# Performance work log

Hardware: AMD Instinct MI355X
Metric: run time of the kernel (lower is better)

The kernel has to match this reference:

```python
import jax, jax.numpy as jnp
import numpy as np

N = 100000   # nodes
E = 1600000  # edges
F = 256      # feature_dim
H = 64       # hidden_dim == out_channels
HEADS = 1


def setup_inputs() -> dict:
    key = jax.random.key(0)
    ks = jax.random.split(key, 12)
    x = jax.random.normal(ks[0], (N, F), dtype=jnp.float32)
    edge_index = jax.random.randint(ks[1], (2, E), 0, N, dtype=jnp.int32)
    s = 0.05
    params = {
        'W_proj': jax.random.normal(ks[2], (F, H), dtype=jnp.float32) * s,
        'b_proj': jnp.zeros((H,), dtype=jnp.float32),
        'Wq1': jax.random.normal(ks[3], (H, HEADS * H), dtype=jnp.float32) * s,
        'Wk1': jax.random.normal(ks[4], (H, HEADS * H), dtype=jnp.float32) * s,
        'Wv1': jax.random.normal(ks[5], (H, HEADS * H), dtype=jnp.float32) * s,
        'Wq2': jax.random.normal(ks[6], (H, HEADS * H), dtype=jnp.float32) * s,
        'Wk2': jax.random.normal(ks[7], (H, HEADS * H), dtype=jnp.float32) * s,
        'Wv2': jax.random.normal(ks[8], (H, HEADS * H), dtype=jnp.float32) * s,
        'W_sig': jax.random.normal(ks[9], (H, 1), dtype=jnp.float32) * s,
        'b_sig': jnp.zeros((1,), dtype=jnp.float32),
    }
    return {'x': x, 'edge_index': edge_index, **params}


def _gat_layer(x, src, dst, Wq, Wk, Wv):
    # x: [N, H]; src/dst: [E] (edge_index[0]=source j, edge_index[1]=dest i)
    n = x.shape[0]
    q = (x @ Wq).reshape(n, HEADS, H)
    k = (x @ Wk).reshape(n, HEADS, H)
    v = (x @ Wv).reshape(n, HEADS, H)
    # edge-wise scores: (q_i * k_j).sum(-1) / sqrt(out_channels)
    scores = jnp.einsum('ehc,ehc->eh', q[dst], k[src]) / np.float32(np.sqrt(H))
    alpha = jax.nn.relu(scores)                                  # [E, HEADS]
    # segment softmax over destination neighborhoods (numerically stable)
    m = jax.ops.segment_max(alpha, dst, num_segments=n)          # [N, HEADS]
    m = jnp.where(jnp.isfinite(m), m, jnp.float32(0.0))
    e = jnp.exp(alpha - m[dst])
    denom = jax.ops.segment_sum(e, dst, num_segments=n)
    a = e / (denom[dst] + jnp.float32(1e-16))                    # [E, HEADS]
    # scatter-weighted sum of values to destinations
    out = jax.ops.segment_sum(v[src] * a[:, :, None], dst, num_segments=n)
    return out.mean(axis=1), a                                   # [N, H], [E, HEADS]


def reference(x, edge_index, W_proj, b_proj, Wq1, Wk1, Wv1, Wq2, Wk2, Wv2, W_sig, b_sig):
    src, dst = edge_index[0], edge_index[1]
    h = jax.nn.gelu(x @ W_proj + b_proj, approximate=False)
    h, attn1 = _gat_layer(h, src, dst, Wq1, Wk1, Wv1)
    h = jax.nn.gelu(h, approximate=False)
    h, attn2 = _gat_layer(h, src, dst, Wq2, Wk2, Wv2)
    signals = h @ W_sig + b_sig                                  # [N, 1]
    return signals, attn1, attn2
```

## Files before the change

### kernel.cpp

```cpp
#include <hip/hip_runtime.h>
#include <hip/hip_fp16.h>
#include <math.h>

#define FF 256
#define HH 64

typedef __attribute__((ext_vector_type(8))) short short8;
typedef __attribute__((ext_vector_type(4))) float f32x4;

__device__ __forceinline__ float gelu_f(float x) {
    float ax = fabsf(x) * 0.70710678118654752f;
    float t = __builtin_amdgcn_rcpf(fmaf(0.3275911f, ax, 1.0f));
    float poly = t * fmaf(t, fmaf(t, fmaf(t, fmaf(t, 1.061405429f, -1.453152027f),
                  1.421413741f), -0.284496736f), 0.254829592f);
    float er = 1.0f - poly * __expf(-ax * ax);
    er = (x < 0.f) ? -er : er;
    return 0.5f * x * (1.0f + er);
}

__device__ __forceinline__ unsigned short bf16rne(float f) {
    unsigned u = __float_as_uint(f);
    unsigned r = u + 0x7FFFu + ((u >> 16) & 1u);
    return (unsigned short)(r >> 16);
}

__device__ __forceinline__ void bf16split(float f, short& hi, short& lo) {
    unsigned u = __float_as_uint(f);
    unsigned r = u + 0x7FFFu + ((u >> 16) & 1u);
    hi = (short)(r >> 16);
    float fh = __uint_as_float(r & 0xFFFF0000u);
    float fl = f - fh;
    unsigned u2 = __float_as_uint(fl);
    unsigned r2 = u2 + 0x7FFFu + ((u2 >> 16) & 1u);
    lo = (short)(r2 >> 16);
}

__device__ __forceinline__ __half2 shfl_xor_h2(__half2 v, int off) {
    union { __half2 h; int i; } u;
    u.h = v;
    u.i = __shfl_xor(u.i, off, 64);
    return u.h;
}

__global__ __launch_bounds__(256) void k_wprep(
        const float* __restrict__ Wp,
        const float* __restrict__ Wq1, const float* __restrict__ Wk1, const float* __restrict__ Wv1,
        const float* __restrict__ Wq2, const float* __restrict__ Wk2, const float* __restrict__ Wv2,
        short* __restrict__ wf) {
    int total = 16384 + 6 * 4096;
    for (int gid = blockIdx.x * 256 + threadIdx.x; gid < total; gid += gridDim.x * 256) {
        const float* W;
        int fid, hibase, lobase;
        if (gid < 16384) {
            W = Wp; fid = gid; hibase = 0; lobase = 16384;
        } else {
            int t = gid - 16384;
            int m = t >> 12;
            fid = t & 4095;
            switch (m) {
                case 0: W = Wq1; break;
                case 1: W = Wk1; break;
                case 2: W = Wv1; break;
                case 3: W = Wq2; break;
                case 4: W = Wk2; break;
                default: W = Wv2; break;
            }
            hibase = 32768 + m * 8192;
            lobase = hibase + 4096;
        }
        int j    = fid & 7;
        int lane = (fid >> 3) & 63;
        int ct   = (fid >> 9) & 3;
        int s    = fid >> 11;
        int k    = s * 32 + (lane >> 4) * 8 + j;
        int col  = ct * 16 + (lane & 15);
        short hi, lo;
        bf16split(W[k * HH + col], hi, lo);
        wf[hibase + fid] = hi;
        wf[lobase + fid] = lo;
    }
}

__global__ __launch_bounds__(256) void k_degree(const int* __restrict__ dst,
        int* __restrict__ deg, int* __restrict__ rank, int E) {
    int e0 = (blockIdx.x * 256 + threadIdx.x) * 4;
    if (e0 + 3 < E) {
        int4 d4 = *reinterpret_cast<const int4*>(dst + e0);
        int4 r4;
        r4.x = atomicAdd(&deg[d4.x], 1);
        r4.y = atomicAdd(&deg[d4.y], 1);
        r4.z = atomicAdd(&deg[d4.z], 1);
        r4.w = atomicAdd(&deg[d4.w], 1);
        *reinterpret_cast<int4*>(rank + e0) = r4;
    } else {
        for (int e = e0; e < E; ++e) rank[e] = atomicAdd(&deg[dst[e]], 1);
    }
}

__global__ __launch_bounds__(256) void k_scan1(const int* __restrict__ deg,
        int* __restrict__ out, int* __restrict__ bsums, int n) {
    __shared__ int lds[256];
    int t = threadIdx.x;
    int base = blockIdx.x * 1024 + t * 4;
    int v0 = (base     < n) ? deg[base]     : 0;
    int v1 = (base + 1 < n) ? deg[base + 1] : 0;
    int v2 = (base + 2 < n) ? deg[base + 2] : 0;
    int v3 = (base + 3 < n) ? deg[base + 3] : 0;
    int s = v0 + v1 + v2 + v3;
    int val = s;
    lds[t] = val;
    __syncthreads();
    #pragma unroll
    for (int off = 1; off < 256; off <<= 1) {
        int tmp = (t >= off) ? lds[t - off] : 0;
        __syncthreads();
        val += tmp;
        lds[t] = val;
        __syncthreads();
    }
    if (t == 255) bsums[blockIdx.x] = val;
    int excl = val - s;
    if (base     < n) out[base]     = excl;
    if (base + 1 < n) out[base + 1] = excl + v0;
    if (base + 2 < n) out[base + 2] = excl + v0 + v1;
    if (base + 3 < n) out[base + 3] = excl + v0 + v1 + v2;
}

__global__ __launch_bounds__(256) void k_scan2(const int* __restrict__ bsums,
        int* __restrict__ boffs, int nb) {
    __shared__ int lds[256];
    int t = threadIdx.x;
    int s = (t < nb) ? bsums[t] : 0;
    int val = s;
    lds[t] = val;
    __syncthreads();
    #pragma unroll
    for (int off = 1; off < 256; off <<= 1) {
        int tmp = (t >= off) ? lds[t - off] : 0;
        __syncthreads();
        val += tmp;
        lds[t] = val;
        __syncthreads();
    }
    if (t < nb) boffs[t] = val - s;
}

__global__ __launch_bounds__(256) void k_scan3(int* __restrict__ rowptr,
        const int* __restrict__ boffs, int n, int E) {
    int i = blockIdx.x * 256 + threadIdx.x;
    if (i < n) rowptr[i] += boffs[i >> 10];
    if (i == n) rowptr[n] = E;
}

__global__ __launch_bounds__(256) void k_fill(const int* __restrict__ src,
        const int* __restrict__ dst, const int* __restrict__ rowptr,
        const int* __restrict__ rank,
        int* __restrict__ esrc, int* __restrict__ inv, int E) {
    int e0 = (blockIdx.x * 256 + threadIdx.x) * 4;
    if (e0 + 3 < E) {
        int4 d4 = *reinterpret_cast<const int4*>(dst + e0);
        int4 s4 = *reinterpret_cast<const int4*>(src + e0);
        int4 r4 = *reinterpret_cast<const int4*>(rank + e0);
        int p0 = rowptr[d4.x] + r4.x;
        int p1 = rowptr[d4.y] + r4.y;
        int p2 = rowptr[d4.z] + r4.z;
        int p3 = rowptr[d4.w] + r4.w;
        esrc[p0] = s4.x;
        esrc[p1] = s4.y;
        esrc[p2] = s4.z;
        esrc[p3] = s4.w;
        *reinterpret_cast<int4*>(inv + e0) = (int4){p0, p1, p2, p3};
    } else {
        for (int e = e0; e < E; ++e) {
            int pos = rowptr[dst[e]] + rank[e];
            esrc[pos] = src[e];
            inv[e] = pos;
        }
    }
}

__global__ __launch_bounds__(256) void k_attn(const float* __restrict__ ecsr,
        const int* __restrict__ inv, float* __restrict__ attn, int E) {
    int e0 = (blockIdx.x * 256 + threadIdx.x) * 4;
    if (e0 + 3 < E) {
        int4 i4 = *reinterpret_cast<const int4*>(inv + e0);
        float4 a;
        a.x = ecsr[i4.x]; a.y = ecsr[i4.y]; a.z = ecsr[i4.z]; a.w = ecsr[i4.w];
        *reinterpret_cast<float4*>(attn + e0) = a;
    } else {
        for (int e = e0; e < E; ++e) attn[e] = ecsr[inv[e]];
    }
}

__global__ __launch_bounds__(256) void k_proj(const float* __restrict__ x,
        const short* __restrict__ wf, const float* __restrict__ b,
        float* __restrict__ h, int n) {
    int lane = threadIdx.x & 63;
    int w    = threadIdx.x >> 6;
    int m    = lane & 15, g = lane >> 4;
    int rowc = min(blockIdx.x * 64 + w * 16 + m, n - 1);
    const float* xrow = x + (size_t)rowc * FF + g * 8;
    const short* wlo = wf + 16384;
    f32x4 acc[4];
    #pragma unroll
    for (int ct = 0; ct < 4; ++ct) acc[ct] = (f32x4){0.f, 0.f, 0.f, 0.f};
    #pragma unroll
    for (int s = 0; s < 8; ++s) {
        float4 a0 = *reinterpret_cast<const float4*>(xrow + s * 32);
        float4 a1 = *reinterpret_cast<const float4*>(xrow + s * 32 + 4);
        float av[8] = {a0.x, a0.y, a0.z, a0.w, a1.x, a1.y, a1.z, a1.w};
        short8 ah, al;
        #pragma unroll
        for (int j = 0; j < 8; ++j) { short hi, lo; bf16split(av[j], hi, lo); ah[j] = hi; al[j] = lo; }
        #pragma unroll
        for (int ct = 0; ct < 4; ++ct) {
            int fo = ((s * 4 + ct) * 64 + lane) * 8;
            short8 bh = *reinterpret_cast<const short8*>(wf + fo);
            short8 bl = *reinterpret_cast<const short8*>(wlo + fo);
            acc[ct] = __builtin_amdgcn_mfma_f32_16x16x32_bf16(ah, bh, acc[ct], 0, 0, 0);
            acc[ct] = __builtin_amdgcn_mfma_f32_16x16x32_bf16(al, bh, acc[ct], 0, 0, 0);
            acc[ct] = __builtin_amdgcn_mfma_f32_16x16x32_bf16(ah, bl, acc[ct], 0, 0, 0);
        }
    }
    int orow0 = blockIdx.x * 64 + w * 16 + g * 4;
    #pragma unroll
    for (int ct = 0; ct < 4; ++ct) {
        int col = ct * 16 + m;
        float bias = b[col];
        #pragma unroll
        for (int r = 0; r < 4; ++r) {
            int row = orow0 + r;
            if (row < n) h[(size_t)row * HH + col] = acc[ct][r] + bias;
        }
    }
}

__global__ __launch_bounds__(256) void k_qkv(const float* __restrict__ hsrc,
        const short* __restrict__ wfq, const short* __restrict__ wfk, const short* __restrict__ wfv,
        __half* __restrict__ qh, __half* __restrict__ kv, int n) {
    int lane = threadIdx.x & 63;
    int w    = threadIdx.x >> 6;
    int m    = lane & 15, g = lane >> 4;
    int rowc = min(blockIdx.x * 64 + w * 16 + m, n - 1);
    const float* hrow = hsrc + (size_t)rowc * HH + g * 8;
    f32x4 aq[4], ak[4], av_[4];
    #pragma unroll
    for (int ct = 0; ct < 4; ++ct) {
        aq[ct] = (f32x4){0.f, 0.f, 0.f, 0.f};
        ak[ct] = (f32x4){0.f, 0.f, 0.f, 0.f};
        av_[ct] = (f32x4){0.f, 0.f, 0.f, 0.f};
    }
    #pragma unroll
    for (int s = 0; s < 2; ++s) {
        float4 a0 = *reinterpret_cast<const float4*>(hrow + s * 32);
        float4 a1 = *reinterpret_cast<const float4*>(hrow + s * 32 + 4);
        float avv[8] = {a0.x, a0.y, a0.z, a0.w, a1.x, a1.y, a1.z, a1.w};
        short8 ah;
        #pragma unroll
        for (int j = 0; j < 8; ++j) ah[j] = (short)bf16rne(gelu_f(avv[j]));
        #pragma unroll
        for (int ct = 0; ct < 4; ++ct) {
            int fo = ((s * 4 + ct) * 64 + lane) * 8;
            short8 qh8 = *reinterpret_cast<const short8*>(wfq + fo);
            short8 ql8 = *reinterpret_cast<const short8*>(wfq + 4096 + fo);
            short8 kh8 = *reinterpret_cast<const short8*>(wfk + fo);
            short8 kl8 = *reinterpret_cast<const short8*>(wfk + 4096 + fo);
            short8 vh8 = *reinterpret_cast<const short8*>(wfv + fo);
            short8 vl8 = *reinterpret_cast<const short8*>(wfv + 4096 + fo);
            aq[ct] = __builtin_amdgcn_mfma_f32_16x16x32_bf16(ah, qh8, aq[ct], 0, 0, 0);
            aq[ct] = __builtin_amdgcn_mfma_f32_16x16x32_bf16(ah, ql8, aq[ct], 0, 0, 0);
            ak[ct] = __builtin_amdgcn_mfma_f32_16x16x32_bf16(ah, kh8, ak[ct], 0, 0, 0);
            ak[ct] = __builtin_amdgcn_mfma_f32_16x16x32_bf16(ah, kl8, ak[ct], 0, 0, 0);
            av_[ct] = __builtin_amdgcn_mfma_f32_16x16x32_bf16(ah, vh8, av_[ct], 0, 0, 0);
            av_[ct] = __builtin_amdgcn_mfma_f32_16x16x32_bf16(ah, vl8, av_[ct], 0, 0, 0);
        }
    }
    int orow0 = blockIdx.x * 64 + w * 16 + g * 4;
    #pragma unroll
    for (int ct = 0; ct < 4; ++ct) {
        int col = ct * 16 + m;
        int cb  = (col >> 3) * 16 + (col & 7);
        #pragma unroll
        for (int r = 0; r < 4; ++r) {
            int row = orow0 + r;
            if (row < n) {
                qh[(size_t)row * HH + col]     = __float2half(aq[ct][r]);
                kv[(size_t)row * 128 + cb]     = __float2half(ak[ct][r]);
                kv[(size_t)row * 128 + cb + 8] = __float2half(av_[ct][r]);
            }
        }
    }
}

template<bool LAST>
__global__ __launch_bounds__(256) void k_edge(
        const __half* __restrict__ qarr, const __half* __restrict__ kv,
        const int* __restrict__ rowptr,
        const int* __restrict__ esrc,
        float* __restrict__ ecsr,
        float* __restrict__ hout,
        float* __restrict__ signals,
        const float* __restrict__ Wsig, const float* __restrict__ bsig,
        int n) {
    int node = blockIdx.x * 4 + (threadIdx.x >> 6);
    if (node >= n) return;
    int lane = threadIdx.x & 63;
    int li = lane & 7, g = lane >> 3;
    int start = rowptr[node], end = rowptr[node + 1];
    int deg = end - start;
    __half2 q2[4];
    {
        union { uint4 u; __half2 h[4]; } Q;
        Q.u = *reinterpret_cast<const uint4*>(qarr + (size_t)node * HH + li * 8);
        #pragma unroll
        for (int j = 0; j < 4; ++j) q2[j] = Q.h[j];
    }
    int p0 = start + lane;
    int el = (p0 < end) ? esrc[p0] : 0;

    __half2 acc2[4];
    #pragma unroll
    for (int j = 0; j < 4; ++j) acc2[j] = __float2half2_rn(0.f);
    float s = 0.f;
    for (int c = 0; c < deg; c += 16) {
        int idx0 = c + g, idx1 = c + 8 + g;
        bool v0 = idx0 < deg, v1 = idx1 < deg;
        int sv0, sv1;
        if (c + 16 <= 64) {
            sv0 = __shfl(el, idx0);
            sv1 = __shfl(el, idx1);
        } else {
            sv0 = v0 ? esrc[start + idx0] : 0;
            sv1 = v1 ? esrc[start + idx1] : 0;
        }
        const __half* b0 = kv + (size_t)sv0 * 128 + li * 16;
        const __half* b1 = kv + (size_t)sv1 * 128 + li * 16;
        union { uint4 u; __half2 h[4]; } K0, V0, K1, V1;
        K0.u = *reinterpret_cast<const uint4*>(b0);
        V0.u = *reinterpret_cast<const uint4*>(b0 + 8);
        K1.u = *reinterpret_cast<const uint4*>(b1);
        V1.u = *reinterpret_cast<const uint4*>(b1 + 8);
        __half2 d20 = __float2half2_rn(0.f);
        __half2 d21 = __float2half2_rn(0.f);
        #pragma unroll
        for (int j = 0; j < 4; ++j) {
            d20 = __hfma2(q2[j], K0.h[j], d20);
            d21 = __hfma2(q2[j], K1.h[j], d21);
        }
        float d0 = __low2float(d20) + __high2float(d20);
        float d1 = __low2float(d21) + __high2float(d21);
        d0 += __shfl_xor(d0, 1); d1 += __shfl_xor(d1, 1);
        d0 += __shfl_xor(d0, 2); d1 += __shfl_xor(d1, 2);
        d0 += __shfl_xor(d0, 4); d1 += __shfl_xor(d1, 4);
        float e0 = v0 ? __expf(fmaxf(d0 * 0.125f, 0.f)) : 0.f;
        float e1 = v1 ? __expf(fmaxf(d1 * 0.125f, 0.f)) : 0.f;
        s += e0 + e1;
        if (v0 && li == 0) ecsr[start + idx0] = e0;
        if (v1 && li == 0) ecsr[start + idx1] = e1;
        __half2 e20 = __float2half2_rn(e0);
        __half2 e21 = __float2half2_rn(e1);
        #pragma unroll
        for (int j = 0; j < 4; ++j) {
            acc2[j] = __hfma2(e20, V0.h[j], acc2[j]);
            acc2[j] = __hfma2(e21, V1.h[j], acc2[j]);
        }
    }
    #pragma unroll
    for (int off = 8; off < 64; off <<= 1) {
        s += __shfl_xor(s, off);
        #pragma unroll
        for (int j = 0; j < 4; ++j)
            acc2[j] = __hadd2(acc2[j], shfl_xor_h2(acc2[j], off));
    }
    float inv = 1.0f / (s + 1e-16f);
    float af[8];
    #pragma unroll
    for (int j = 0; j < 4; ++j) {
        af[2 * j]     = __low2float(acc2[j]);
        af[2 * j + 1] = __high2float(acc2[j]);
    }

    if (!LAST) {
        if (g == 0) {
            float4 o0, o1;
            o0.x = af[0] * inv; o0.y = af[1] * inv; o0.z = af[2] * inv; o0.w = af[3] * inv;
            o1.x = af[4] * inv; o1.y = af[5] * inv; o1.z = af[6] * inv; o1.w = af[7] * inv;
            *reinterpret_cast<float4*>(hout + (size_t)node * HH + li * 8)     = o0;
            *reinterpret_cast<float4*>(hout + (size_t)node * HH + li * 8 + 4) = o1;
        }
    } else {
        float4 w0 = *reinterpret_cast<const float4*>(Wsig + li * 8);
        float4 w1 = *reinterpret_cast<const float4*>(Wsig + li * 8 + 4);
        float t = af[0] * w0.x + af[1] * w0.y + af[2] * w0.z + af[3] * w0.w
                + af[4] * w1.x + af[5] * w1.y + af[6] * w1.z + af[7] * w1.w;
        t *= inv;
        t += __shfl_xor(t, 1);
        t += __shfl_xor(t, 2);
        t += __shfl_xor(t, 4);
        if (lane == 0) signals[node] = t + bsig[0];
    }
    for (int p = p0; p < end; p += 64)
        ecsr[p] *= inv;
}

extern "C" void kernel_launch(void* const* d_in, const int* in_sizes, int n_in,
                              void* d_out, int out_size, void* d_ws, size_t ws_size,
                              hipStream_t stream) {
    const float* x   = (const float*)d_in[0];
    const int*   ei  = (const int*)  d_in[1];
    const float* Wp  = (const float*)d_in[2];
    const float* bp  = (const float*)d_in[3];
    const float* Wq1 = (const float*)d_in[4];
    const float* Wk1 = (const float*)d_in[5];
    const float* Wv1 = (const float*)d_in[6];
    const float* Wq2 = (const float*)d_in[7];
    const float* Wk2 = (const float*)d_in[8];
    const float* Wv2 = (const float*)d_in[9];
    const float* Wsg = (const float*)d_in[10];
    const float* bsg = (const float*)d_in[11];

    const int N = in_sizes[0] / FF;
    const int E = in_sizes[1] / 2;
    const int* src = ei;
    const int* dst = ei + E;

    char* ws = (char*)d_ws;
    size_t off = 0;
    auto alloc = [&](size_t bytes) -> void* {
        void* p = ws + off;
        off += (bytes + 255) & ~(size_t)255;
        return p;
    };
    __half* qh   = (__half*)alloc((size_t)N * HH * 2);
    __half* kv   = (__half*)alloc((size_t)N * 128 * 2);
    float* h     = (float*)alloc((size_t)N * HH * 4);
    float* ecsr  = (float*)alloc((size_t)E * 4);
    int* inv     = (int*)alloc((size_t)E * 4);
    int* esrc    = (int*)alloc((size_t)E * 4);
    int* rank    = (int*)alloc((size_t)E * 4);
    int* deg     = (int*)alloc((size_t)N * 4);
    int* rowptr  = (int*)alloc((size_t)(N + 1) * 4);
    int* bsums   = (int*)alloc(256 * 4);
    int* boffs   = (int*)alloc(256 * 4);
    short* wf    = (short*)alloc((size_t)81920 * 2);

    float* out     = (float*)d_out;
    float* signals = out;
    float* attn1   = out + N;
    float* attn2   = out + N + E;

    k_wprep<<<64, 256, 0, stream>>>(Wp, Wq1, Wk1, Wv1, Wq2, Wk2, Wv2, wf);

    hipMemsetAsync(deg, 0, (size_t)N * 4, stream);
    int e4Blocks = ((E + 3) / 4 + 255) / 256;
    k_degree<<<e4Blocks, 256, 0, stream>>>(dst, deg, rank, E);
    int nb = (N + 1023) / 1024;
    k_scan1<<<nb, 256, 0, stream>>>(deg, rowptr, bsums, N);
    k_scan2<<<1, 256, 0, stream>>>(bsums, boffs, nb);
    k_scan3<<<(N + 1 + 255) / 256, 256, 0, stream>>>(rowptr, boffs, N, E);
    k_fill<<<e4Blocks, 256, 0, stream>>>(src, dst, rowptr, rank, esrc, inv, E);

    int gemmBlocks = (N + 63) / 64;

    k_proj<<<gemmBlocks, 256, 0, stream>>>(x, wf, bp, h, N);

    const short* wfbase = wf + 32768;
    k_qkv<<<gemmBlocks, 256, 0, stream>>>(h, wfbase, wfbase + 8192, wfbase + 16384,
            qh, kv, N);
    k_edge<false><<<(N + 3) / 4, 256, 0, stream>>>(qh, kv, rowptr, esrc,
            ecsr, h, nullptr, nullptr, nullptr, N);
    k_attn<<<e4Blocks, 256, 0, stream>>>(ecsr, inv, attn1, E);

    k_qkv<<<gemmBlocks, 256, 0, stream>>>(h, wfbase + 24576, wfbase + 32768, wfbase + 40960,
            qh, kv, N);
    k_edge<true><<<(N + 3) / 4, 256, 0, stream>>>(qh, kv, rowptr, esrc,
            ecsr, nullptr, signals, Wsg, bsg, N);
    k_attn<<<e4Blocks, 256, 0, stream>>>(ecsr, inv, attn2, E);
}
```

Before: 341.5 us.

## Fuse independent GEMM and edge-index kernels into shared launches via block interleaving

Merges the projection GEMM with degree counting, the first QKV GEMM with the CSR fill, and the second QKV GEMM with the first attention scatter into single launches, with even blocks doing GEMM work and odd blocks doing edge work. This removes three kernel launches and lets compute-bound MFMA blocks overlap with memory-bound atomic/gather blocks. The fused kernels take the register usage of the heavier branch, which may reduce occupancy for the lightweight edge blocks.

Result: faster. 304.2 us (-10.9%).

```diff
diff --git a/kernel.cpp b/kernel.cpp
--- a/kernel.cpp
+++ b/kernel.cpp
@@ -81,9 +81,9 @@
     }
 }
 
-__global__ __launch_bounds__(256) void k_degree(const int* __restrict__ dst,
+__device__ __forceinline__ void do_degree(int bid, const int* __restrict__ dst,
         int* __restrict__ deg, int* __restrict__ rank, int E) {
-    int e0 = (blockIdx.x * 256 + threadIdx.x) * 4;
+    int e0 = (bid * 256 + threadIdx.x) * 4;
     if (e0 + 3 < E) {
         int4 d4 = *reinterpret_cast<const int4*>(dst + e0);
         int4 r4;
@@ -97,66 +97,11 @@
     }
 }
 
-__global__ __launch_bounds__(256) void k_scan1(const int* __restrict__ deg,
-        int* __restrict__ out, int* __restrict__ bsums, int n) {
-    __shared__ int lds[256];
-    int t = threadIdx.x;
-    int base = blockIdx.x * 1024 + t * 4;
-    int v0 = (base     < n) ? deg[base]     : 0;
-    int v1 = (base + 1 < n) ? deg[base + 1] : 0;
-    int v2 = (base + 2 < n) ? deg[base + 2] : 0;
-    int v3 = (base + 3 < n) ? deg[base + 3] : 0;
-    int s = v0 + v1 + v2 + v3;
-    int val = s;
-    lds[t] = val;
-    __syncthreads();
-    #pragma unroll
-    for (int off = 1; off < 256; off <<= 1) {
-        int tmp = (t >= off) ? lds[t - off] : 0;
-        __syncthreads();
-        val += tmp;
-        lds[t] = val;
-        __syncthreads();
-    }
-    if (t == 255) bsums[blockIdx.x] = val;
-    int excl = val - s;
-    if (base     < n) out[base]     = excl;
-    if (base + 1 < n) out[base + 1] = excl + v0;
-    if (base + 2 < n) out[base + 2] = excl + v0 + v1;
-    if (base + 3 < n) out[base + 3] = excl + v0 + v1 + v2;
-}
-
-__global__ __launch_bounds__(256) void k_scan2(const int* __restrict__ bsums,
-        int* __restrict__ boffs, int nb) {
-    __shared__ int lds[256];
-    int t = threadIdx.x;
-    int s = (t < nb) ? bsums[t] : 0;
-    int val = s;
-    lds[t] = val;
-    __syncthreads();
-    #pragma unroll
-    for (int off = 1; off < 256; off <<= 1) {
-        int tmp = (t >= off) ? lds[t - off] : 0;
-        __syncthreads();
-        val += tmp;
-        lds[t] = val;
-        __syncthreads();
-    }
-    if (t < nb) boffs[t] = val - s;
-}
-
-__global__ __launch_bounds__(256) void k_scan3(int* __restrict__ rowptr,
-        const int* __restrict__ boffs, int n, int E) {
-    int i = blockIdx.x * 256 + threadIdx.x;
-    if (i < n) rowptr[i] += boffs[i >> 10];
-    if (i == n) rowptr[n] = E;
-}
-
-__global__ __launch_bounds__(256) void k_fill(const int* __restrict__ src,
+__device__ __forceinline__ void do_fill(int bid, const int* __restrict__ src,
         const int* __restrict__ dst, const int* __restrict__ rowptr,
         const int* __restrict__ rank,
         int* __restrict__ esrc, int* __restrict__ inv, int E) {
-    int e0 = (blockIdx.x * 256 + threadIdx.x) * 4;
+    int e0 = (bid * 256 + threadIdx.x) * 4;
     if (e0 + 3 < E) {
         int4 d4 = *reinterpret_cast<const int4*>(dst + e0);
         int4 s4 = *reinterpret_cast<const int4*>(src + e0);
@@ -179,9 +124,9 @@
     }
 }
 
-__global__ __launch_bounds__(256) void k_attn(const float* __restrict__ ecsr,
+__device__ __forceinline__ void do_attn(int bid, const float* __restrict__ ecsr,
         const int* __restrict__ inv, float* __restrict__ attn, int E) {
-    int e0 = (blockIdx.x * 256 + threadIdx.x) * 4;
+    int e0 = (bid * 256 + threadIdx.x) * 4;
     if (e0 + 3 < E) {
         int4 i4 = *reinterpret_cast<const int4*>(inv + e0);
         float4 a;
@@ -192,13 +137,14 @@
     }
 }
 
-__global__ __launch_bounds__(256) void k_proj(const float* __restrict__ x,
+__device__ __forceinline__ void do_proj(int bid, const float* __restrict__ x,
         const short* __restrict__ wf, const float* __restrict__ b,
         float* __restrict__ h, int n) {
+    if (bid * 64 >= n) return;
     int lane = threadIdx.x & 63;
     int w    = threadIdx.x >> 6;
     int m    = lane & 15, g = lane >> 4;
-    int rowc = min(blockIdx.x * 64 + w * 16 + m, n - 1);
+    int rowc = min(bid * 64 + w * 16 + m, n - 1);
     const float* xrow = x + (size_t)rowc * FF + g * 8;
     const short* wlo = wf + 16384;
     f32x4 acc[4];
@@ -222,7 +168,7 @@
             acc[ct] = __builtin_amdgcn_mfma_f32_16x16x32_bf16(ah, bl, acc[ct], 0, 0, 0);
         }
     }
-    int orow0 = blockIdx.x * 64 + w * 16 + g * 4;
+    int orow0 = bid * 64 + w * 16 + g * 4;
     #pragma unroll
     for (int ct = 0; ct < 4; ++ct) {
         int col = ct * 16 + m;
@@ -235,13 +181,14 @@
     }
 }
 
-__global__ __launch_bounds__(256) void k_qkv(const float* __restrict__ hsrc,
+__device__ __forceinline__ void do_qkv(int bid, const float* __restrict__ hsrc,
         const short* __restrict__ wfq, const short* __restrict__ wfk, const short* __restrict__ wfv,
         __half* __restrict__ qh, __half* __restrict__ kv, int n) {
+    if (bid * 64 >= n) return;
     int lane = threadIdx.x & 63;
     int w    = threadIdx.x >> 6;
     int m    = lane & 15, g = lane >> 4;
-    int rowc = min(blockIdx.x * 64 + w * 16 + m, n - 1);
+    int rowc = min(bid * 64 + w * 16 + m, n - 1);
     const float* hrow = hsrc + (size_t)rowc * HH + g * 8;
     f32x4 aq[4], ak[4], av_[4];
     #pragma unroll
@@ -275,7 +222,7 @@
             av_[ct] = __builtin_amdgcn_mfma_f32_16x16x32_bf16(ah, vl8, av_[ct], 0, 0, 0);
         }
     }
-    int orow0 = blockIdx.x * 64 + w * 16 + g * 4;
+    int orow0 = bid * 64 + w * 16 + g * 4;
     #pragma unroll
     for (int ct = 0; ct < 4; ++ct) {
         int col = ct * 16 + m;
@@ -290,6 +237,98 @@
             }
         }
     }
+}
+
+__global__ __launch_bounds__(256) void k_proj_degree(
+        const float* __restrict__ x, const short* __restrict__ wf,
+        const float* __restrict__ b, float* __restrict__ h, int n,
+        const int* __restrict__ dst, int* __restrict__ deg, int* __restrict__ rank, int E) {
+    int bid = blockIdx.x >> 1;
+    if ((blockIdx.x & 1) == 0) do_proj(bid, x, wf, b, h, n);
+    else                       do_degree(bid, dst, deg, rank, E);
+}
+
+__global__ __launch_bounds__(256) void k_qkv_fill(
+        const float* __restrict__ hsrc,
+        const short* __restrict__ wfq, const short* __restrict__ wfk, const short* __restrict__ wfv,
+        __half* __restrict__ qh, __half* __restrict__ kv, int n,
+        const int* __restrict__ src, const int* __restrict__ dst,
+        const int* __restrict__ rowptr, const int* __restrict__ rank,
+        int* __restrict__ esrc, int* __restrict__ inv, int E) {
+    int bid = blockIdx.x >> 1;
+    if ((blockIdx.x & 1) == 0) do_qkv(bid, hsrc, wfq, wfk, wfv, qh, kv, n);
+    else                       do_fill(bid, src, dst, rowptr, rank, esrc, inv, E);
+}
+
+__global__ __launch_bounds__(256) void k_qkv_attn(
+        const float* __restrict__ hsrc,
+        const short* __restrict__ wfq, const short* __restrict__ wfk, const short* __restrict__ wfv,
+        __half* __restrict__ qh, __half* __restrict__ kv, int n,
+        const float* __restrict__ ecsr, const int* __restrict__ inv,
+        float* __restrict__ attn, int E) {
+    int bid = blockIdx.x >> 1;
+    if ((blockIdx.x & 1) == 0) do_qkv(bid, hsrc, wfq, wfk, wfv, qh, kv, n);
+    else                       do_attn(bid, ecsr, inv, attn, E);
+}
+
+__global__ __launch_bounds__(256) void k_attn(const float* __restrict__ ecsr,
+        const int* __restrict__ inv, float* __restrict__ attn, int E) {
+    do_attn(blockIdx.x, ecsr, inv, attn, E);
+}
+
+__global__ __launch_bounds__(256) void k_scan1(const int* __restrict__ deg,
+        int* __restrict__ out, int* __restrict__ bsums, int n) {
+    __shared__ int lds[256];
+    int t = threadIdx.x;
+    int base = blockIdx.x * 1024 + t * 4;
+    int v0 = (base     < n) ? deg[base]     : 0;
+    int v1 = (base + 1 < n) ? deg[base + 1] : 0;
+    int v2 = (base + 2 < n) ? deg[base + 2] : 0;
+    int v3 = (base + 3 < n) ? deg[base + 3] : 0;
+    int s = v0 + v1 + v2 + v3;
+    int val = s;
+    lds[t] = val;
+    __syncthreads();
+    #pragma unroll
+    for (int off = 1; off < 256; off <<= 1) {
+        int tmp = (t >= off) ? lds[t - off] : 0;
+        __syncthreads();
+        val += tmp;
+        lds[t] = val;
+        __syncthreads();
+    }
+    if (t == 255) bsums[blockIdx.x] = val;
+    int excl = val - s;
+    if (base     < n) out[base]     = excl;
+    if (base + 1 < n) out[base + 1] = excl + v0;
+    if (base + 2 < n) out[base + 2] = excl + v0 + v1;
+    if (base + 3 < n) out[base + 3] = excl + v0 + v1 + v2;
+}
+
+__global__ __launch_bounds__(256) void k_scan2(const int* __restrict__ bsums,
+        int* __restrict__ boffs, int nb) {
+    __shared__ int lds[256];
+    int t = threadIdx.x;
+    int s = (t < nb) ? bsums[t] : 0;
+    int val = s;
+    lds[t] = val;
+    __syncthreads();
+    #pragma unroll
+    for (int off = 1; off < 256; off <<= 1) {
+        int tmp = (t >= off) ? lds[t - off] : 0;
+        __syncthreads();
+        val += tmp;
+        lds[t] = val;
+        __syncthreads();
+    }
+    if (t < nb) boffs[t] = val - s;
+}
+
+__global__ __launch_bounds__(256) void k_scan3(int* __restrict__ rowptr,
+        const int* __restrict__ boffs, int n, int E) {
+    int i = blockIdx.x * 256 + threadIdx.x;
+    if (i < n) rowptr[i] += boffs[i >> 10];
+    if (i == n) rowptr[n] = E;
 }
 
 template<bool LAST>
@@ -450,29 +489,27 @@
     float* attn2   = out + N + E;
 
     k_wprep<<<64, 256, 0, stream>>>(Wp, Wq1, Wk1, Wv1, Wq2, Wk2, Wv2, wf);
-
     hipMemsetAsync(deg, 0, (size_t)N * 4, stream);
-    int e4Blocks = ((E + 3) / 4 + 255) / 256;
-    k_degree<<<e4Blocks, 256, 0, stream>>>(dst, deg, rank, E);
+
+    int gemmBlocks = (N + 63) / 64;
+    int e4Blocks   = ((E + 3) / 4 + 255) / 256;
+    int fused1     = 2 * max(gemmBlocks, e4Blocks);
+
+    k_proj_degree<<<fused1, 256, 0, stream>>>(x, wf, bp, h, N, dst, deg, rank, E);
+
     int nb = (N + 1023) / 1024;
     k_scan1<<<nb, 256, 0, stream>>>(deg, rowptr, bsums, N);
     k_scan2<<<1, 256, 0, stream>>>(bsums, boffs, nb);
     k_scan3<<<(N + 1 + 255) / 256, 256, 0, stream>>>(rowptr, boffs, N, E);
-    k_fill<<<e4Blocks, 256, 0, stream>>>(src, dst, rowptr, rank, esrc, inv, E);
-
-    int gemmBlocks = (N + 63) / 64;
-
-    k_proj<<<gemmBlocks, 256, 0, stream>>>(x, wf, bp, h, N);
 
     const short* wfbase = wf + 32768;
-    k_qkv<<<gemmBlocks, 256, 0, stream>>>(h, wfbase, wfbase + 8192, wfbase + 16384,
-            qh, kv, N);
+    k_qkv_fill<<<fused1, 256, 0, stream>>>(h, wfbase, wfbase + 8192, wfbase + 16384,
+            qh, kv, N, src, dst, rowptr, rank, esrc, inv, E);
     k_edge<false><<<(N + 3) / 4, 256, 0, stream>>>(qh, kv, rowptr, esrc,
             ecsr, h, nullptr, nullptr, nullptr, N);
-    k_attn<<<e4Blocks, 256, 0, stream>>>(ecsr, inv, attn1, E);
-
-    k_qkv<<<gemmBlocks, 256, 0, stream>>>(h, wfbase + 24576, wfbase + 32768, wfbase + 40960,
-            qh, kv, N);
+
+    k_qkv_attn<<<fused1, 256, 0, stream>>>(h, wfbase + 24576, wfbase + 32768, wfbase + 40960,
+            qh, kv, N, ecsr, inv, attn1, E);
     k_edge<true><<<(N + 3) / 4, 256, 0, stream>>>(qh, kv, rowptr, esrc,
             ecsr, nullptr, signals, Wsg, bsg, N);
     k_attn<<<e4Blocks, 256, 0, stream>>>(ecsr, inv, attn2, E);
```
